# Kernel tuning notes

Hardware: AMD Instinct MI355X
Metric: run time of the kernel (lower is better)

## Reference

```python
import jax, jax.numpy as jnp
import numpy as np

DIM = 128

def setup_inputs() -> dict:
    key = jax.random.key(0)
    k1, k2, k3, k4, k5, k6 = jax.random.split(key, 6)
    bs = 16
    n_nodes = 65536  # bs * 4096 nodes per graph
    n_edges = 500000
    node_features = jax.random.normal(k1, (n_nodes, DIM), dtype=jnp.float32)
    edge_index = jax.random.randint(k2, (2, n_edges), 0, n_nodes, dtype=jnp.int64)
    centroid = jax.random.normal(k3, (bs, DIM), dtype=jnp.float32)
    # MLP params: Linear(3*dim, dim) -> ReLU -> (Dropout eval=identity) -> Linear(dim, 1)
    lim1 = 1.0 / np.sqrt(3 * DIM)
    W1 = jax.random.uniform(k4, (3 * DIM, DIM), minval=-lim1, maxval=lim1, dtype=jnp.float32)
    b1 = jnp.zeros((DIM,), dtype=jnp.float32)
    lim2 = 1.0 / np.sqrt(DIM)
    W2 = jax.random.uniform(k5, (DIM, 1), minval=-lim2, maxval=lim2, dtype=jnp.float32)
    b2 = jnp.zeros((1,), dtype=jnp.float32)
    return {"node_features": node_features, "edge_index": edge_index, "centroid": centroid,
            "bs": bs, "W1": W1, "b1": b1, "W2": W2, "b2": b2}

def reference(node_features, edge_index, centroid, bs, W1, b1, W2, b2):
    # node_features: [N, dim]; edge_index: [2, E]; centroid: [bs, dim]
    nf = node_features.reshape(-1, DIM)
    node_j = nf[edge_index[0]]  # [E, dim]
    node_i = nf[edge_index[1]]  # [E, dim]
    # residual = node_features - per-graph centroid
    residual = (nf.reshape(bs, -1, DIM) - centroid.reshape(bs, 1, DIM)).reshape(-1, DIM)
    res_j = residual[edge_index[0]]
    res_i = residual[edge_index[1]]
    sim_vec = jnp.concatenate([jnp.abs(node_i - node_j), res_i, res_j], axis=1)  # [E, 3*dim]
    h = jax.nn.relu(sim_vec @ W1 + b1)  # dropout is identity in eval mode
    prob_score = h @ W2 + b2  # [E, 1]
    return prob_score
```

## Files before the change

### kernel.cpp

```cpp
#include <hip/hip_runtime.h>
#include <hip/hip_bf16.h>
#include <stdint.h>

#define DIM 128
#define ITERS 8

typedef __attribute__((ext_vector_type(8))) short short8;
typedef __attribute__((ext_vector_type(4))) short s16x4;
typedef __attribute__((ext_vector_type(4))) float f32x4;
typedef __attribute__((ext_vector_type(8))) unsigned short ushort8;

__device__ __forceinline__ float bf2f(unsigned short u) {
    unsigned int x = ((unsigned int)u) << 16;
    return __builtin_bit_cast(float, x);
}
__device__ __forceinline__ unsigned short f2bf(float f) {
    unsigned int x = __builtin_bit_cast(unsigned int, f);
    x += 0x7fffu + ((x >> 16) & 1u);
    return (unsigned short)(x >> 16);
}

__global__ void prep_weights(const float* __restrict__ W1,
                             unsigned short* __restrict__ W1bcT,
                             unsigned short* __restrict__ packA) {
    int t = blockIdx.x * 256 + threadIdx.x;
    if (t < 256 * 128) {
        int c = t >> 7, k = t & 127;
        int row = 128 + ((c >> 7) << 7) + k;
        W1bcT[t] = f2bf(W1[row * DIM + (c & 127)]);
    } else {
        int o = t - 256 * 128;
        int x = o & 7, l = (o >> 3) & 63, o2 = o >> 9;
        int s = o2 & 3, T = o2 >> 2;
        int col = T * 16 + (l & 15);
        int k = s * 32 + (l >> 4) * 8 + x;
        packA[o] = f2bf(W1[k * DIM + col]);
    }
}

__global__ __launch_bounds__(512) void precompute_PQ(
    const float* __restrict__ nf, const float* __restrict__ centroid,
    const unsigned short* __restrict__ W1bcT, const float* __restrict__ b1,
    unsigned short* __restrict__ nf16, unsigned short* __restrict__ PQ, int npg)
{
    __shared__ char sA[64 * 256];
    const int t = threadIdx.x;
    const int n0 = blockIdx.x * 64;

    {
        int row = t >> 3;
        int c0 = (t & 7) * 16;
        int n = n0 + row;
        int g = n / npg;
        const f32x4* nv = (const f32x4*)(nf + (size_t)n * DIM + c0);
        const f32x4* cv = (const f32x4*)(centroid + (size_t)g * DIM + c0);
        unsigned short sh[16];
        ushort8 raw[2];
#pragma unroll
        for (int u = 0; u < 4; ++u) {
            f32x4 a = nv[u], c = cv[u];
#pragma unroll
            for (int x = 0; x < 4; ++x) {
                raw[u >> 1][(u & 1) * 4 + x] = f2bf(a[x]);
                sh[u * 4 + x] = f2bf(a[x] - c[x]);
            }
        }
        *(ushort8*)(nf16 + (size_t)n * DIM + c0)     = raw[0];
        *(ushort8*)(nf16 + (size_t)n * DIM + c0 + 8) = raw[1];
#pragma unroll
        for (int v = 0; v < 2; ++v) {
            int inrow = c0 * 2 + v * 16;
            int phys = row * 256 + (inrow ^ ((row & 7) << 4));
            *(short8*)(sA + phys) = *(const short8*)(sh + v * 8);
        }
    }

    const int wid = t >> 6, l = t & 63, lo = l & 15, hi = l >> 4;
    const int wm = wid & 1, wn = wid >> 1;

    short8 B[4][4];
#pragma unroll
    for (int nt = 0; nt < 4; ++nt) {
        int row = wn * 64 + nt * 16 + lo;
        const short8* wp = (const short8*)(W1bcT + (size_t)row * DIM + hi * 8);
#pragma unroll
        for (int kk = 0; kk < 4; ++kk) B[nt][kk] = wp[kk * 4];
    }

    __syncthreads();

    f32x4 acc[2][4];
#pragma unroll
    for (int mt = 0; mt < 2; ++mt)
#pragma unroll
        for (int nt = 0; nt < 4; ++nt) acc[mt][nt] = (f32x4)0.0f;

#pragma unroll
    for (int kk = 0; kk < 4; ++kk) {
        short8 a[2];
#pragma unroll
        for (int mt = 0; mt < 2; ++mt) {
            int row = wm * 32 + mt * 16 + lo;
            int inrow = kk * 64 + hi * 16;
            int phys = row * 256 + (inrow ^ ((row & 7) << 4));
            a[mt] = *(const short8*)(sA + phys);
        }
#pragma unroll
        for (int mt = 0; mt < 2; ++mt)
#pragma unroll
            for (int nt = 0; nt < 4; ++nt)
                acc[mt][nt] = __builtin_amdgcn_mfma_f32_16x16x32_bf16(
                    a[mt], B[nt][kk], acc[mt][nt], 0, 0, 0);
    }

#pragma unroll
    for (int nt = 0; nt < 4; ++nt) {
        int col = wn * 64 + nt * 16 + lo;
        float bb = (col < DIM) ? b1[col] : 0.0f;
#pragma unroll
        for (int mt = 0; mt < 2; ++mt)
#pragma unroll
            for (int q = 0; q < 4; ++q) {
                int n = n0 + wm * 32 + mt * 16 + hi * 4 + q;
                PQ[(size_t)n * 256 + col] = f2bf(acc[mt][nt][q] + bb);
            }
    }
}

__device__ __forceinline__ void stage_convert_write(
    char* sD, unsigned short* sS, int e, int c0,
    ushort8 a0, ushort8 a1, ushort8 b0, ushort8 b1,
    ushort8 P0, ushort8 P1, ushort8 Q0, ushort8 Q1)
{
    unsigned short d[16];
    unsigned short s[16];
#pragma unroll
    for (int x = 0; x < 8; ++x) {
        d[x]     = f2bf(fabsf(bf2f(a0[x]) - bf2f(b0[x])));
        d[8 + x] = f2bf(fabsf(bf2f(a1[x]) - bf2f(b1[x])));
        s[x]     = f2bf(bf2f(P0[x]) + bf2f(Q0[x]));
        s[8 + x] = f2bf(bf2f(P1[x]) + bf2f(Q1[x]));
    }
    int rs = e * 256, sw = (e & 7) << 4, inb = c0 * 2;
    *(short8*)(sD + rs + ((inb     ) ^ sw)) = *(const short8*)d;
    *(short8*)(sD + rs + ((inb + 16) ^ sw)) = *(const short8*)(d + 8);
    unsigned short* base = sS + e * 132 + c0;
#pragma unroll
    for (int u = 0; u < 4; ++u)
        *(s16x4*)(base + u * 4) = *(const s16x4*)(s + u * 4);
}

__global__ __launch_bounds__(256, 4) void edge_kernel(
    const unsigned short* __restrict__ nf16, const int* __restrict__ idx,
    const unsigned short* __restrict__ PQ, const unsigned short* __restrict__ packA,
    const float* __restrict__ W2, const float* __restrict__ b2,
    float* __restrict__ out, int E, int nTiles)
{
    __shared__ char  sD[32 * 256];
    __shared__ unsigned short sS[32 * 132];
    __shared__ float sR[4][32];
    const int t = threadIdx.x;
    const int l = t & 63, wn = t >> 6, lo = l & 15, hi = l >> 4;
    const int es = t >> 3, c0 = (t & 7) * 16;

    short8 B[2][4];
    {
        const short8* bp = (const short8*)packA;
#pragma unroll
        for (int nt = 0; nt < 2; ++nt)
#pragma unroll
            for (int kk = 0; kk < 4; ++kk)
                B[nt][kk] = bp[((wn * 2 + nt) * 4 + kk) * 64 + l];
    }
    float w2v[2];
    w2v[0] = W2[wn * 32 + lo];
    w2v[1] = W2[wn * 32 + 16 + lo];
    const float b2v = b2[0];

    const int tile0 = blockIdx.x * ITERS;
    const int nT = min(ITERS, nTiles - tile0);

    {
        int ge = tile0 * 32 + es;
        int jj = idx[ge], ii = idx[E + ge];
        const ushort8* pi = (const ushort8*)(nf16 + (size_t)ii * DIM + c0);
        const ushort8* pj = (const ushort8*)(nf16 + (size_t)jj * DIM + c0);
        const ushort8* Pp = (const ushort8*)(PQ + (size_t)ii * 256 + c0);
        const ushort8* Qp = (const ushort8*)(PQ + (size_t)jj * 256 + DIM + c0);
        stage_convert_write(sD, sS, es, c0, pi[0], pi[1], pj[0], pj[1],
                            Pp[0], Pp[1], Qp[0], Qp[1]);
    }
    ushort8 pA0, pA1, pB0, pB1, pP0, pP1, pQ0, pQ1;
    int ii_n, jj_n;
    {
        int t1 = min(tile0 + 1, nTiles - 1);
        int ge = t1 * 32 + es;
        int jj = idx[ge], ii = idx[E + ge];
        const ushort8* pi = (const ushort8*)(nf16 + (size_t)ii * DIM + c0);
        const ushort8* pj = (const ushort8*)(nf16 + (size_t)jj * DIM + c0);
        const ushort8* Pp = (const ushort8*)(PQ + (size_t)ii * 256 + c0);
        const ushort8* Qp = (const ushort8*)(PQ + (size_t)jj * 256 + DIM + c0);
        pA0 = pi[0]; pA1 = pi[1]; pB0 = pj[0]; pB1 = pj[1];
        pP0 = Pp[0]; pP1 = Pp[1]; pQ0 = Qp[0]; pQ1 = Qp[1];
        int t2 = min(tile0 + 2, nTiles - 1);
        int ge2 = t2 * 32 + es;
        jj_n = idx[ge2]; ii_n = idx[E + ge2];
    }
    __syncthreads();

    for (int tt = 0; tt < nT; ++tt) {
        f32x4 acc[2][2];
#pragma unroll
        for (int mt = 0; mt < 2; ++mt)
#pragma unroll
            for (int nt = 0; nt < 2; ++nt) acc[mt][nt] = (f32x4)0.0f;

#pragma unroll
        for (int kk = 0; kk < 4; ++kk) {
            short8 a[2];
#pragma unroll
            for (int mt = 0; mt < 2; ++mt) {
                int row = mt * 16 + lo;
                int inrow = kk * 64 + hi * 16;
                a[mt] = *(const short8*)(sD + row * 256 + (inrow ^ ((row & 7) << 4)));
            }
#pragma unroll
            for (int mt = 0; mt < 2; ++mt)
#pragma unroll
                for (int nt = 0; nt < 2; ++nt)
                    acc[mt][nt] = __builtin_amdgcn_mfma_f32_16x16x32_bf16(
                        a[mt], B[nt][kk], acc[mt][nt], 0, 0, 0);
        }

#pragma unroll
        for (int mt = 0; mt < 2; ++mt)
#pragma unroll
            for (int q = 0; q < 4; ++q) {
                int el = mt * 16 + hi * 4 + q;
                float s = 0.0f;
#pragma unroll
                for (int nt = 0; nt < 2; ++nt) {
                    int col = wn * 32 + nt * 16 + lo;
                    float h = acc[mt][nt][q] + bf2f(sS[el * 132 + col]);
                    s += fmaxf(h, 0.0f) * w2v[nt];
                }
                s += __shfl_xor(s, 1);
                s += __shfl_xor(s, 2);
                s += __shfl_xor(s, 4);
                s += __shfl_xor(s, 8);
                if (lo == 0) sR[wn][el] = s;
            }
        __syncthreads();

        {
            int ge = (tile0 + tt) * 32 + t;
            if (t < 32 && ge < E)
                out[ge] = sR[0][t] + sR[1][t] + sR[2][t] + sR[3][t] + b2v;
        }

        if (tt + 1 < nT) {
            stage_convert_write(sD, sS, es, c0, pA0, pA1, pB0, pB1,
                                pP0, pP1, pQ0, pQ1);
            {
                const ushort8* pi = (const ushort8*)(nf16 + (size_t)ii_n * DIM + c0);
                const ushort8* pj = (const ushort8*)(nf16 + (size_t)jj_n * DIM + c0);
                const ushort8* Pp = (const ushort8*)(PQ + (size_t)ii_n * 256 + c0);
                const ushort8* Qp = (const ushort8*)(PQ + (size_t)jj_n * 256 + DIM + c0);
                pA0 = pi[0]; pA1 = pi[1]; pB0 = pj[0]; pB1 = pj[1];
                pP0 = Pp[0]; pP1 = Pp[1]; pQ0 = Qp[0]; pQ1 = Qp[1];
            }
            {
                int t3 = min(tile0 + tt + 3, nTiles - 1);
                int ge3 = t3 * 32 + es;
                jj_n = idx[ge3]; ii_n = idx[E + ge3];
            }
        }
        __syncthreads();
    }
}

extern "C" void kernel_launch(void* const* d_in, const int* in_sizes, int n_in,
                              void* d_out, int out_size, void* d_ws, size_t ws_size,
                              hipStream_t stream) {
    const float* nf       = (const float*)d_in[0];
    const int*   idx      = (const int*)d_in[1];
    const float* centroid = (const float*)d_in[2];
    const float* W1       = (const float*)d_in[4];
    const float* b1       = (const float*)d_in[5];
    const float* W2       = (const float*)d_in[6];
    const float* b2       = (const float*)d_in[7];
    float* out = (float*)d_out;

    const int n_nodes = in_sizes[0] / DIM;
    const int E       = in_sizes[1] / 2;
    const int bs      = in_sizes[2] / DIM;
    const int npg     = n_nodes / bs;

    unsigned short* nf16  = (unsigned short*)d_ws;
    unsigned short* PQ    = nf16 + (size_t)n_nodes * DIM;
    unsigned short* W1bcT = PQ + (size_t)n_nodes * 256;
    unsigned short* packA = W1bcT + 256 * 128;

    prep_weights<<<192, 256, 0, stream>>>(W1, W1bcT, packA);
    precompute_PQ<<<n_nodes / 64, 512, 0, stream>>>(nf, centroid, W1bcT, b1,
                                                    nf16, PQ, npg);
    int nTiles = (E + 31) / 32;
    edge_kernel<<<(nTiles + ITERS - 1) / ITERS, 256, 0, stream>>>(
        nf16, idx, PQ, packA, W2, b2, out, E, nTiles);
}
```

Baseline: 189.4 us.

## Double edge-kernel block to 512 threads with one N-tile per wave

Moves the edge kernel from 256 to 512 threads per block. Each of the 8 waves now owns a single 16-column slice of the hidden layer, and each thread gathers 8 features per edge instead of 16. This halves per-thread registers and memory requests, giving more waves in flight to hide gather latency, and raises launch bounds to 8 blocks. In exchange there are more partial sums to reduce through shared memory and more block-wide syncs, and edge indices are now clamped against E.

```diff
diff --git a/kernel.cpp b/kernel.cpp
--- a/kernel.cpp
+++ b/kernel.cpp
@@ -128,29 +128,23 @@
 }
 
 __device__ __forceinline__ void stage_convert_write(
-    char* sD, unsigned short* sS, int e, int c0,
-    ushort8 a0, ushort8 a1, ushort8 b0, ushort8 b1,
-    ushort8 P0, ushort8 P1, ushort8 Q0, ushort8 Q1)
+    char* sD, unsigned short* sS, int e, int q,
+    ushort8 a, ushort8 b, ushort8 P, ushort8 Q)
 {
-    unsigned short d[16];
-    unsigned short s[16];
+    unsigned short d[8], s[8];
 #pragma unroll
     for (int x = 0; x < 8; ++x) {
-        d[x]     = f2bf(fabsf(bf2f(a0[x]) - bf2f(b0[x])));
-        d[8 + x] = f2bf(fabsf(bf2f(a1[x]) - bf2f(b1[x])));
-        s[x]     = f2bf(bf2f(P0[x]) + bf2f(Q0[x]));
-        s[8 + x] = f2bf(bf2f(P1[x]) + bf2f(Q1[x]));
-    }
-    int rs = e * 256, sw = (e & 7) << 4, inb = c0 * 2;
-    *(short8*)(sD + rs + ((inb     ) ^ sw)) = *(const short8*)d;
-    *(short8*)(sD + rs + ((inb + 16) ^ sw)) = *(const short8*)(d + 8);
-    unsigned short* base = sS + e * 132 + c0;
-#pragma unroll
-    for (int u = 0; u < 4; ++u)
-        *(s16x4*)(base + u * 4) = *(const s16x4*)(s + u * 4);
-}
-
-__global__ __launch_bounds__(256, 4) void edge_kernel(
+        d[x] = f2bf(fabsf(bf2f(a[x]) - bf2f(b[x])));
+        s[x] = f2bf(bf2f(P[x]) + bf2f(Q[x]));
+    }
+    int phys = e * 256 + ((q * 16) ^ ((e & 7) << 4));
+    *(short8*)(sD + phys) = *(const short8*)d;
+    unsigned short* base = sS + e * 132 + q * 8;
+    *(s16x4*)(base)     = *(const s16x4*)(s);
+    *(s16x4*)(base + 4) = *(const s16x4*)(s + 4);
+}
+
+__global__ __launch_bounds__(512, 8) void edge_kernel(
     const unsigned short* __restrict__ nf16, const int* __restrict__ idx,
     const unsigned short* __restrict__ PQ, const unsigned short* __restrict__ packA,
     const float* __restrict__ W2, const float* __restrict__ b2,
@@ -158,120 +152,97 @@
 {
     __shared__ char  sD[32 * 256];
     __shared__ unsigned short sS[32 * 132];
-    __shared__ float sR[4][32];
+    __shared__ float sR[8][32];
     const int t = threadIdx.x;
-    const int l = t & 63, wn = t >> 6, lo = l & 15, hi = l >> 4;
-    const int es = t >> 3, c0 = (t & 7) * 16;
-
-    short8 B[2][4];
+    const int l = t & 63, wr = t >> 6, lo = l & 15, hi = l >> 4;
+    const int es = t >> 4, qc = t & 15;
+
+    short8 B[4];
     {
         const short8* bp = (const short8*)packA;
 #pragma unroll
-        for (int nt = 0; nt < 2; ++nt)
-#pragma unroll
-            for (int kk = 0; kk < 4; ++kk)
-                B[nt][kk] = bp[((wn * 2 + nt) * 4 + kk) * 64 + l];
-    }
-    float w2v[2];
-    w2v[0] = W2[wn * 32 + lo];
-    w2v[1] = W2[wn * 32 + 16 + lo];
+        for (int kk = 0; kk < 4; ++kk)
+            B[kk] = bp[(wr * 4 + kk) * 64 + l];
+    }
+    const float w2v = W2[wr * 16 + lo];
     const float b2v = b2[0];
 
     const int tile0 = blockIdx.x * ITERS;
     const int nT = min(ITERS, nTiles - tile0);
 
     {
-        int ge = tile0 * 32 + es;
+        int ge = min(tile0 * 32 + es, E - 1);
         int jj = idx[ge], ii = idx[E + ge];
-        const ushort8* pi = (const ushort8*)(nf16 + (size_t)ii * DIM + c0);
-        const ushort8* pj = (const ushort8*)(nf16 + (size_t)jj * DIM + c0);
-        const ushort8* Pp = (const ushort8*)(PQ + (size_t)ii * 256 + c0);
-        const ushort8* Qp = (const ushort8*)(PQ + (size_t)jj * 256 + DIM + c0);
-        stage_convert_write(sD, sS, es, c0, pi[0], pi[1], pj[0], pj[1],
-                            Pp[0], Pp[1], Qp[0], Qp[1]);
-    }
-    ushort8 pA0, pA1, pB0, pB1, pP0, pP1, pQ0, pQ1;
+        const ushort8* pa = (const ushort8*)(nf16 + (size_t)ii * DIM + qc * 8);
+        const ushort8* pb = (const ushort8*)(nf16 + (size_t)jj * DIM + qc * 8);
+        const ushort8* pp = (const ushort8*)(PQ + (size_t)ii * 256 + qc * 8);
+        const ushort8* pq = (const ushort8*)(PQ + (size_t)jj * 256 + DIM + qc * 8);
+        stage_convert_write(sD, sS, es, qc, pa[0], pb[0], pp[0], pq[0]);
+    }
+    ushort8 pA, pB, pP, pQ;
     int ii_n, jj_n;
     {
         int t1 = min(tile0 + 1, nTiles - 1);
-        int ge = t1 * 32 + es;
+        int ge = min(t1 * 32 + es, E - 1);
         int jj = idx[ge], ii = idx[E + ge];
-        const ushort8* pi = (const ushort8*)(nf16 + (size_t)ii * DIM + c0);
-        const ushort8* pj = (const ushort8*)(nf16 + (size_t)jj * DIM + c0);
-        const ushort8* Pp = (const ushort8*)(PQ + (size_t)ii * 256 + c0);
-        const ushort8* Qp = (const ushort8*)(PQ + (size_t)jj * 256 + DIM + c0);
-        pA0 = pi[0]; pA1 = pi[1]; pB0 = pj[0]; pB1 = pj[1];
-        pP0 = Pp[0]; pP1 = Pp[1]; pQ0 = Qp[0]; pQ1 = Qp[1];
+        pA = *(const ushort8*)(nf16 + (size_t)ii * DIM + qc * 8);
+        pB = *(const ushort8*)(nf16 + (size_t)jj * DIM + qc * 8);
+        pP = *(const ushort8*)(PQ + (size_t)ii * 256 + qc * 8);
+        pQ = *(const ushort8*)(PQ + (size_t)jj * 256 + DIM + qc * 8);
         int t2 = min(tile0 + 2, nTiles - 1);
-        int ge2 = t2 * 32 + es;
+        int ge2 = min(t2 * 32 + es, E - 1);
         jj_n = idx[ge2]; ii_n = idx[E + ge2];
     }
     __syncthreads();
 
     for (int tt = 0; tt < nT; ++tt) {
-        f32x4 acc[2][2];
+        f32x4 acc[2];
+        acc[0] = (f32x4)0.0f;
+        acc[1] = (f32x4)0.0f;
+#pragma unroll
+        for (int kk = 0; kk < 4; ++kk) {
+            int inrow = kk * 64 + hi * 16;
+            int r0 = lo, r1 = 16 + lo;
+            short8 a0 = *(const short8*)(sD + r0 * 256 + (inrow ^ ((r0 & 7) << 4)));
+            short8 a1 = *(const short8*)(sD + r1 * 256 + (inrow ^ ((r1 & 7) << 4)));
+            acc[0] = __builtin_amdgcn_mfma_f32_16x16x32_bf16(a0, B[kk], acc[0], 0, 0, 0);
+            acc[1] = __builtin_amdgcn_mfma_f32_16x16x32_bf16(a1, B[kk], acc[1], 0, 0, 0);
+        }
+
 #pragma unroll
         for (int mt = 0; mt < 2; ++mt)
 #pragma unroll
-            for (int nt = 0; nt < 2; ++nt) acc[mt][nt] = (f32x4)0.0f;
-
-#pragma unroll
-        for (int kk = 0; kk < 4; ++kk) {
-            short8 a[2];
-#pragma unroll
-            for (int mt = 0; mt < 2; ++mt) {
-                int row = mt * 16 + lo;
-                int inrow = kk * 64 + hi * 16;
-                a[mt] = *(const short8*)(sD + row * 256 + (inrow ^ ((row & 7) << 4)));
-            }
-#pragma unroll
-            for (int mt = 0; mt < 2; ++mt)
-#pragma unroll
-                for (int nt = 0; nt < 2; ++nt)
-                    acc[mt][nt] = __builtin_amdgcn_mfma_f32_16x16x32_bf16(
-                        a[mt], B[nt][kk], acc[mt][nt], 0, 0, 0);
-        }
-
-#pragma unroll
-        for (int mt = 0; mt < 2; ++mt)
-#pragma unroll
-            for (int q = 0; q < 4; ++q) {
-                int el = mt * 16 + hi * 4 + q;
-                float s = 0.0f;
-#pragma unroll
-                for (int nt = 0; nt < 2; ++nt) {
-                    int col = wn * 32 + nt * 16 + lo;
-                    float h = acc[mt][nt][q] + bf2f(sS[el * 132 + col]);
-                    s += fmaxf(h, 0.0f) * w2v[nt];
-                }
+            for (int qd = 0; qd < 4; ++qd) {
+                int el = mt * 16 + hi * 4 + qd;
+                float h = acc[mt][qd] + bf2f(sS[el * 132 + wr * 16 + lo]);
+                float s = fmaxf(h, 0.0f) * w2v;
                 s += __shfl_xor(s, 1);
                 s += __shfl_xor(s, 2);
                 s += __shfl_xor(s, 4);
                 s += __shfl_xor(s, 8);
-                if (lo == 0) sR[wn][el] = s;
+                if (lo == 0) sR[wr][el] = s;
             }
         __syncthreads();
 
         {
             int ge = (tile0 + tt) * 32 + t;
-            if (t < 32 && ge < E)
-                out[ge] = sR[0][t] + sR[1][t] + sR[2][t] + sR[3][t] + b2v;
+            if (t < 32 && ge < E) {
+                float v = b2v;
+#pragma unroll
+                for (int w = 0; w < 8; ++w) v += sR[w][t];
+                out[ge] = v;
+            }
         }
 
         if (tt + 1 < nT) {
-            stage_convert_write(sD, sS, es, c0, pA0, pA1, pB0, pB1,
-                                pP0, pP1, pQ0, pQ1);
-            {
-                const ushort8* pi = (const ushort8*)(nf16 + (size_t)ii_n * DIM + c0);
-                const ushort8* pj = (const ushort8*)(nf16 + (size_t)jj_n * DIM + c0);
-                const ushort8* Pp = (const ushort8*)(PQ + (size_t)ii_n * 256 + c0);
-                const ushort8* Qp = (const ushort8*)(PQ + (size_t)jj_n * 256 + DIM + c0);
-                pA0 = pi[0]; pA1 = pi[1]; pB0 = pj[0]; pB1 = pj[1];
-                pP0 = Pp[0]; pP1 = Pp[1]; pQ0 = Qp[0]; pQ1 = Qp[1];
-            }
+            stage_convert_write(sD, sS, es, qc, pA, pB, pP, pQ);
+            pA = *(const ushort8*)(nf16 + (size_t)ii_n * DIM + qc * 8);
+            pB = *(const ushort8*)(nf16 + (size_t)jj_n * DIM + qc * 8);
+            pP = *(const ushort8*)(PQ + (size_t)ii_n * 256 + qc * 8);
+            pQ = *(const ushort8*)(PQ + (size_t)jj_n * 256 + DIM + qc * 8);
             {
                 int t3 = min(tile0 + tt + 3, nTiles - 1);
-                int ge3 = t3 * 32 + es;
+                int ge3 = min(t3 * 32 + es, E - 1);
                 jj_n = idx[ge3]; ii_n = idx[E + ge3];
             }
         }
@@ -305,6 +276,6 @@
     precompute_PQ<<<n_nodes / 64, 512, 0, stream>>>(nf, centroid, W1bcT, b1,
                                                     nf16, PQ, npg);
     int nTiles = (E + 31) / 32;
-    edge_kernel<<<(nTiles + ITERS - 1) / ITERS, 256, 0, stream>>>(
+    edge_kernel<<<(nTiles + ITERS - 1) / ITERS, 512, 0, stream>>>(
         nf16, idx, PQ, packA, W2, b2, out, E, nTiles);
 }
```

Result: slower. 231.0 us (+22.0%).

## Interleave bf16 node features and P/Q projections into one per-node row

Applied to the files above, without the earlier changes.

Merges the separate nf16 and PQ buffers into a single 384-element row per node (features, P, Q), so each edge gather for a node touches one contiguous region rather than two separate arrays. The precompute kernel now stages its P/Q outputs through shared memory and writes them as coalesced vector rows instead of scattered 2-byte stores. Edge index reads are also clamped to E-1 so the tail tile does not read past the index array. The extra LDS staging and a second barrier add some cost to the precompute kernel.

```diff
diff --git a/kernel.cpp b/kernel.cpp
--- a/kernel.cpp
+++ b/kernel.cpp
@@ -4,6 +4,7 @@
 
 #define DIM 128
 #define ITERS 8
+#define CSTRIDE 384
 
 typedef __attribute__((ext_vector_type(8))) short short8;
 typedef __attribute__((ext_vector_type(4))) short s16x4;
@@ -38,12 +39,12 @@
     }
 }
 
-__global__ __launch_bounds__(512) void precompute_PQ(
+__global__ __launch_bounds__(512) void precompute_C(
     const float* __restrict__ nf, const float* __restrict__ centroid,
     const unsigned short* __restrict__ W1bcT, const float* __restrict__ b1,
-    unsigned short* __restrict__ nf16, unsigned short* __restrict__ PQ, int npg)
+    unsigned short* __restrict__ C, int npg)
 {
-    __shared__ char sA[64 * 256];
+    __shared__ char sBuf[64 * 512];
     const int t = threadIdx.x;
     const int n0 = blockIdx.x * 64;
 
@@ -65,13 +66,13 @@
                 sh[u * 4 + x] = f2bf(a[x] - c[x]);
             }
         }
-        *(ushort8*)(nf16 + (size_t)n * DIM + c0)     = raw[0];
-        *(ushort8*)(nf16 + (size_t)n * DIM + c0 + 8) = raw[1];
+        *(ushort8*)(C + (size_t)n * CSTRIDE + c0)     = raw[0];
+        *(ushort8*)(C + (size_t)n * CSTRIDE + c0 + 8) = raw[1];
 #pragma unroll
         for (int v = 0; v < 2; ++v) {
             int inrow = c0 * 2 + v * 16;
             int phys = row * 256 + (inrow ^ ((row & 7) << 4));
-            *(short8*)(sA + phys) = *(const short8*)(sh + v * 8);
+            *(short8*)(sBuf + phys) = *(const short8*)(sh + v * 8);
         }
     }
 
@@ -103,7 +104,7 @@
             int row = wm * 32 + mt * 16 + lo;
             int inrow = kk * 64 + hi * 16;
             int phys = row * 256 + (inrow ^ ((row & 7) << 4));
-            a[mt] = *(const short8*)(sA + phys);
+            a[mt] = *(const short8*)(sBuf + phys);
         }
 #pragma unroll
         for (int mt = 0; mt < 2; ++mt)
@@ -113,17 +114,29 @@
                     a[mt], B[nt][kk], acc[mt][nt], 0, 0, 0);
     }
 
+    __syncthreads();
+
+    unsigned short* sOut = (unsigned short*)sBuf;
 #pragma unroll
     for (int nt = 0; nt < 4; ++nt) {
         int col = wn * 64 + nt * 16 + lo;
         float bb = (col < DIM) ? b1[col] : 0.0f;
 #pragma unroll
-        for (int mt = 0; mt < 2; ++mt)
-#pragma unroll
-            for (int q = 0; q < 4; ++q) {
-                int n = n0 + wm * 32 + mt * 16 + hi * 4 + q;
-                PQ[(size_t)n * 256 + col] = f2bf(acc[mt][nt][q] + bb);
-            }
+        for (int mt = 0; mt < 2; ++mt) {
+            int rb = wm * 32 + mt * 16 + hi * 4;
+#pragma unroll
+            for (int q = 0; q < 4; ++q)
+                sOut[(rb + q) * 256 + col] = f2bf(acc[mt][nt][q] + bb);
+        }
+    }
+    __syncthreads();
+
+    {
+        int row = t >> 3, seg = t & 7;
+        const s16x4* src = (const s16x4*)(sOut + row * 256 + seg * 32);
+        s16x4* dst = (s16x4*)(C + (size_t)(n0 + row) * CSTRIDE + DIM + seg * 32);
+#pragma unroll
+        for (int u = 0; u < 8; ++u) dst[u] = src[u];
     }
 }
 
@@ -151,8 +164,8 @@
 }
 
 __global__ __launch_bounds__(256, 4) void edge_kernel(
-    const unsigned short* __restrict__ nf16, const int* __restrict__ idx,
-    const unsigned short* __restrict__ PQ, const unsigned short* __restrict__ packA,
+    const unsigned short* __restrict__ C, const int* __restrict__ idx,
+    const unsigned short* __restrict__ packA,
     const float* __restrict__ W2, const float* __restrict__ b2,
     float* __restrict__ out, int E, int nTiles)
 {
@@ -181,12 +194,12 @@
     const int nT = min(ITERS, nTiles - tile0);
 
     {
-        int ge = tile0 * 32 + es;
+        int ge = min(tile0 * 32 + es, E - 1);
         int jj = idx[ge], ii = idx[E + ge];
-        const ushort8* pi = (const ushort8*)(nf16 + (size_t)ii * DIM + c0);
-        const ushort8* pj = (const ushort8*)(nf16 + (size_t)jj * DIM + c0);
-        const ushort8* Pp = (const ushort8*)(PQ + (size_t)ii * 256 + c0);
-        const ushort8* Qp = (const ushort8*)(PQ + (size_t)jj * 256 + DIM + c0);
+        const ushort8* pi = (const ushort8*)(C + (size_t)ii * CSTRIDE + c0);
+        const ushort8* pj = (const ushort8*)(C + (size_t)jj * CSTRIDE + c0);
+        const ushort8* Pp = (const ushort8*)(C + (size_t)ii * CSTRIDE + DIM + c0);
+        const ushort8* Qp = (const ushort8*)(C + (size_t)jj * CSTRIDE + 2 * DIM + c0);
         stage_convert_write(sD, sS, es, c0, pi[0], pi[1], pj[0], pj[1],
                             Pp[0], Pp[1], Qp[0], Qp[1]);
     }
@@ -194,16 +207,16 @@
     int ii_n, jj_n;
     {
         int t1 = min(tile0 + 1, nTiles - 1);
-        int ge = t1 * 32 + es;
+        int ge = min(t1 * 32 + es, E - 1);
         int jj = idx[ge], ii = idx[E + ge];
-        const ushort8* pi = (const ushort8*)(nf16 + (size_t)ii * DIM + c0);
-        const ushort8* pj = (const ushort8*)(nf16 + (size_t)jj * DIM + c0);
-        const ushort8* Pp = (const ushort8*)(PQ + (size_t)ii * 256 + c0);
-        const ushort8* Qp = (const ushort8*)(PQ + (size_t)jj * 256 + DIM + c0);
+        const ushort8* pi = (const ushort8*)(C + (size_t)ii * CSTRIDE + c0);
+        const ushort8* pj = (const ushort8*)(C + (size_t)jj * CSTRIDE + c0);
+        const ushort8* Pp = (const ushort8*)(C + (size_t)ii * CSTRIDE + DIM + c0);
+        const ushort8* Qp = (const ushort8*)(C + (size_t)jj * CSTRIDE + 2 * DIM + c0);
         pA0 = pi[0]; pA1 = pi[1]; pB0 = pj[0]; pB1 = pj[1];
         pP0 = Pp[0]; pP1 = Pp[1]; pQ0 = Qp[0]; pQ1 = Qp[1];
         int t2 = min(tile0 + 2, nTiles - 1);
-        int ge2 = t2 * 32 + es;
+        int ge2 = min(t2 * 32 + es, E - 1);
         jj_n = idx[ge2]; ii_n = idx[E + ge2];
     }
     __syncthreads();
@@ -262,16 +275,16 @@
             stage_convert_write(sD, sS, es, c0, pA0, pA1, pB0, pB1,
                                 pP0, pP1, pQ0, pQ1);
             {
-                const ushort8* pi = (const ushort8*)(nf16 + (size_t)ii_n * DIM + c0);
-                const ushort8* pj = (const ushort8*)(nf16 + (size_t)jj_n * DIM + c0);
-                const ushort8* Pp = (const ushort8*)(PQ + (size_t)ii_n * 256 + c0);
-                const ushort8* Qp = (const ushort8*)(PQ + (size_t)jj_n * 256 + DIM + c0);
+                const ushort8* pi = (const ushort8*)(C + (size_t)ii_n * CSTRIDE + c0);
+                const ushort8* pj = (const ushort8*)(C + (size_t)jj_n * CSTRIDE + c0);
+                const ushort8* Pp = (const ushort8*)(C + (size_t)ii_n * CSTRIDE + DIM + c0);
+                const ushort8* Qp = (const ushort8*)(C + (size_t)jj_n * CSTRIDE + 2 * DIM + c0);
                 pA0 = pi[0]; pA1 = pi[1]; pB0 = pj[0]; pB1 = pj[1];
                 pP0 = Pp[0]; pP1 = Pp[1]; pQ0 = Qp[0]; pQ1 = Qp[1];
             }
             {
                 int t3 = min(tile0 + tt + 3, nTiles - 1);
-                int ge3 = t3 * 32 + es;
+                int ge3 = min(t3 * 32 + es, E - 1);
                 jj_n = idx[ge3]; ii_n = idx[E + ge3];
             }
         }
@@ -296,15 +309,14 @@
     const int bs      = in_sizes[2] / DIM;
     const int npg     = n_nodes / bs;
 
-    unsigned short* nf16  = (unsigned short*)d_ws;
-    unsigned short* PQ    = nf16 + (size_t)n_nodes * DIM;
-    unsigned short* W1bcT = PQ + (size_t)n_nodes * 256;
+    unsigned short* C     = (unsigned short*)d_ws;
+    unsigned short* W1bcT = C + (size_t)n_nodes * CSTRIDE;
     unsigned short* packA = W1bcT + 256 * 128;
 
     prep_weights<<<192, 256, 0, stream>>>(W1, W1bcT, packA);
-    precompute_PQ<<<n_nodes / 64, 512, 0, stream>>>(nf, centroid, W1bcT, b1,
-                                                    nf16, PQ, npg);
+    precompute_C<<<n_nodes / 64, 512, 0, stream>>>(nf, centroid, W1bcT, b1,
+                                                   C, npg);
     int nTiles = (E + 31) / 32;
     edge_kernel<<<(nTiles + ITERS - 1) / ITERS, 256, 0, stream>>>(
-        nf16, idx, PQ, packA, W2, b2, out, E, nTiles);
-}
+        C, idx, packA, W2, b2, out, E, nTiles);
+}
```

Result: slower. 195.4 us (+3.2%).
